# Optimization experiments

Hardware: AMD Instinct MI355X
Metric: run time of the kernel (lower is better)

Reference implementation:

```python
import jax, jax.numpy as jnp
import numpy as np

N_PATHS = 100000
N_STEPS = 512          # number of Euler steps; paths have N_STEPS+1 time points
DT = 0.004             # step_size (~1/250, daily)
KAPPA = 1.0
THETA = 0.04
SIGMA = 0.2
RHO = -0.7
S0 = 100.0
V0 = 0.04


def setup_inputs() -> dict:
    key = jax.random.key(0)
    z = jax.random.normal(key, (N_PATHS, N_STEPS, 2), dtype=jnp.float32)
    return {"z": z}


def reference(z):
    # Euler-Maruyama simulation of the Heston SDE with full-truncation clamp:
    #   dS = S * sqrt(v) dW1
    #   dv = kappa*(theta - v) dt + sigma*sqrt(v) dW2,  corr(dW1,dW2)=rho
    sqdt = jnp.sqrt(jnp.float32(DT))
    c = jnp.sqrt(jnp.float32(1.0 - RHO * RHO))

    def step(carry, zt):
        s, v = carry                      # each [N]
        vp = jnp.maximum(v, 0.0)
        sv = jnp.sqrt(vp)
        dW1 = sqdt * zt[:, 0]
        dW2 = RHO * dW1 + c * sqdt * zt[:, 1]
        s_new = s + s * sv * dW1
        v_new = jnp.maximum(v + KAPPA * (THETA - vp) * DT + SIGMA * sv * dW2, 0.0)
        return (s_new, v_new), (s_new, v_new)

    s0 = jnp.full((N_PATHS,), S0, dtype=z.dtype)
    v0 = jnp.full((N_PATHS,), V0, dtype=z.dtype)
    _, (ss, vs) = jax.lax.scan(step, (s0, v0), jnp.transpose(z, (1, 0, 2)))

    prices = jnp.concatenate([s0[None], ss], axis=0).T      # [N, T+1]
    variances = jnp.concatenate([v0[None], vs], axis=0).T   # [N, T+1]

    # variance-swap price: cumsum of variance * dt + analytic remaining leg L
    tau = jnp.linspace(N_STEPS * DT, 0.0, N_STEPS + 1).astype(z.dtype)  # [T+1]
    L = (variances - THETA) / KAPPA * (1.0 - jnp.exp(-KAPPA * tau)) + THETA * tau
    varswap = jnp.cumsum(variances, axis=1) * DT + L        # [N, T+1]

    # [N, T+1, 3] = (price, variance, varswap price)
    return jnp.stack([prices, variances, varswap], axis=-1)
```

## Files before the change

### kernel.cpp

```cpp
#include <hip/hip_runtime.h>
#include <hip/hip_fp16.h>


#define N_PATHS 100000
#define N_STEPS 512
#define TROW    1539
#define PB      64
#define SUB     16
#define NSUB    32
#define NPH     8
#define PHSUB   4
#define OSTR    97
#define DTc     0.004f
#define EDT     1.0040080107f

typedef float  f32x4  __attribute__((ext_vector_type(4)));
typedef __fp16 fp16x2 __attribute__((ext_vector_type(2)));

__device__ __forceinline__ unsigned pk2(float a, float b) {
    union { fp16x2 h; unsigned u; } cv;
    cv.h = __builtin_amdgcn_cvt_pkrtz(a, b);
    return cv.u;
}

__device__ __forceinline__ float ex16(unsigned w, int h) {
    const unsigned us = h ? (w >> 16) : (w & 0xFFFFu);
    return __half2float(__ushort_as_half((unsigned short)us));
}

__global__ __launch_bounds__(PB)
void heston_kernel(const float* __restrict__ z, float* __restrict__ out) {
    __shared__ unsigned olB[PB * OSTR];

    const int tid = threadIdx.x;
    const int p0  = blockIdx.x * PB;
    const int lim = N_PATHS - p0;
    const int limS = (lim >= PB) ? PB : lim;
    const int p   = p0 + tid;
    const int pc  = (p < N_PATHS) ? p : (N_PATHS - 1);

    const char* zp = (const char*)z + (size_t)pc * 4096;

    f32x4 fA[8], fB[8];
    #pragma unroll
    for (int j = 0; j < 8; ++j) fA[j] = *(const f32x4*)(zp + 16 * j);

    {
        #pragma unroll
        for (int k = 0; k < 3; ++k) {
            int idx = k * PB + tid;
            int pl = idx / 3, si = idx - pl * 3;
            if (pl < lim)
                out[(size_t)(p0 + pl) * TROW + si] =
                    (si == 0) ? 100.0f : (si == 1) ? 0.04f : 0.08208f;
        }
    }

    float s = 100.0f, v = 0.04f, acc = 0.04f, tau = 2.048f, e = expf(-2.048f);
    float sP = 0.f, vP = 0.f, vsP = 0.f;

    auto doSub = [&](int sc, int su, f32x4 (&cur)[8], f32x4 (&nxt)[8]) {
        if (sc + 1 < NSUB) {
            const char* zc = zp + (size_t)(sc + 1) * 128;
            #pragma unroll
            for (int j = 0; j < 8; ++j) nxt[j] = *(const f32x4*)(zc + 16 * j);
        }
        const int dbase = tid * OSTR + su * 24;
        #pragma unroll
        for (int dt = 0; dt < SUB; ++dt) {
            const f32x4 q  = cur[dt >> 1];
            const float z0 = (dt & 1) ? q.z : q.x;
            const float z1 = (dt & 1) ? q.w : q.y;

            const float vp  = fmaxf(v, 0.0f);
            const float sv  = __builtin_amdgcn_sqrtf(vp);
            const float dW1 = 0.06324555320f * z0;
            const float dW2 = fmaf(-0.7f, dW1, 0.04516636050f * z1);
            s = fmaf(s * sv, dW1, s);
            v = fmaxf(fmaf(0.2f * sv, dW2, fmaf(0.04f - vp, DTc, v)), 0.0f);
            acc += v;
            tau -= DTc;
            e *= EDT;
            const float vs = fmaf(acc, DTc, fmaf(0.04f, tau, (v - 0.04f) * (1.0f - e)));

            if (dt & 1) {
                const int d = dbase + 3 * (dt >> 1);
                olB[d + 0] = pk2(sP, vP);
                olB[d + 1] = pk2(vsP, s);
                olB[d + 2] = pk2(v, vs);
            } else { sP = s; vP = v; vsP = vs; }
        }
    };

    const int h  = tid & 1;
    const int tq = tid >> 1;

    for (int ph = 0; ph < NPH; ++ph) {
        const int sc0 = ph * PHSUB;
        doSub(sc0 + 0, 0, fA, fB);
        doSub(sc0 + 1, 1, fB, fA);
        doSub(sc0 + 2, 2, fA, fB);
        doSub(sc0 + 3, 3, fB, fA);

        float* gp = out + (size_t)p0 * TROW + 3 + ph * 192;
        if (limS == PB) {
            for (int pl = 0; pl < PB; ++pl) {
                const unsigned* lw = &olB[pl * OSTR + tq];
                float* gr = gp + (size_t)pl * TROW + tid;
                gr[0]   = ex16(lw[0],  h);
                gr[64]  = ex16(lw[32], h);
                gr[128] = ex16(lw[64], h);
            }
        } else {
            for (int pl = 0; pl < limS; ++pl) {
                const unsigned* lw = &olB[pl * OSTR + tq];
                float* gr = gp + (size_t)pl * TROW + tid;
                gr[0]   = ex16(lw[0],  h);
                gr[64]  = ex16(lw[32], h);
                gr[128] = ex16(lw[64], h);
            }
        }
    }
}

extern "C" void kernel_launch(void* const* d_in, const int* in_sizes, int n_in,
                              void* d_out, int out_size, void* d_ws, size_t ws_size,
                              hipStream_t stream) {
    const float* z = (const float*)d_in[0];
    float* out = (float*)d_out;
    const int nblocks = (N_PATHS + PB - 1) / PB;
    heston_kernel<<<nblocks, PB, 0, stream>>>(z, out);
}
```

Measured before the change: 328.2 us.

## Buffer full path trajectories in LDS and emit contiguous float4 output stores

Each block now simulates 48 paths, with 16 idle lanes in a 64-thread block, and stores the whole trajectory of s, v and varswap as fp16 in three shared-memory planes. After the simulation it writes the block's contiguous output region with float4 coalesced stores, rather than eight phases of strided scalar row writes. The aim is fully contiguous, wide global writes for the large output. The cost is about 148KB of LDS per block, which limits occupancy to about one block per CU. It also adds per-element index math (division by 3, row wrap), and the compute and store phases no longer overlap.

```diff
diff --git a/kernel.cpp b/kernel.cpp
--- a/kernel.cpp
+++ b/kernel.cpp
@@ -5,39 +5,28 @@
 #define N_PATHS 100000
 #define N_STEPS 512
 #define TROW    1539
+#define PPB     48
 #define PB      64
 #define SUB     16
 #define NSUB    32
-#define NPH     8
-#define PHSUB   4
-#define OSTR    97
+#define HSTR    513
 #define DTc     0.004f
 #define EDT     1.0040080107f
 
-typedef float  f32x4  __attribute__((ext_vector_type(4)));
-typedef __fp16 fp16x2 __attribute__((ext_vector_type(2)));
-
-__device__ __forceinline__ unsigned pk2(float a, float b) {
-    union { fp16x2 h; unsigned u; } cv;
-    cv.h = __builtin_amdgcn_cvt_pkrtz(a, b);
-    return cv.u;
-}
-
-__device__ __forceinline__ float ex16(unsigned w, int h) {
-    const unsigned us = h ? (w >> 16) : (w & 0xFFFFu);
-    return __half2float(__ushort_as_half((unsigned short)us));
-}
+typedef float f32x4 __attribute__((ext_vector_type(4)));
 
 __global__ __launch_bounds__(PB)
 void heston_kernel(const float* __restrict__ z, float* __restrict__ out) {
-    __shared__ unsigned olB[PB * OSTR];
+    __shared__ _Float16 S_l[PPB * HSTR];
+    __shared__ _Float16 V_l[PPB * HSTR];
+    __shared__ _Float16 W_l[PPB * HSTR];
 
     const int tid = threadIdx.x;
-    const int p0  = blockIdx.x * PB;
-    const int lim = N_PATHS - p0;
-    const int limS = (lim >= PB) ? PB : lim;
-    const int p   = p0 + tid;
-    const int pc  = (p < N_PATHS) ? p : (N_PATHS - 1);
+    const int p0  = blockIdx.x * PPB;
+    const int lim = (N_PATHS - p0 < PPB) ? (N_PATHS - p0) : PPB;
+    const bool act = (tid < PPB);
+    const int  pp  = p0 + tid;
+    const int  pc  = (pp < N_PATHS) ? pp : (N_PATHS - 1);
 
     const char* zp = (const char*)z + (size_t)pc * 4096;
 
@@ -45,27 +34,15 @@
     #pragma unroll
     for (int j = 0; j < 8; ++j) fA[j] = *(const f32x4*)(zp + 16 * j);
 
-    {
-        #pragma unroll
-        for (int k = 0; k < 3; ++k) {
-            int idx = k * PB + tid;
-            int pl = idx / 3, si = idx - pl * 3;
-            if (pl < lim)
-                out[(size_t)(p0 + pl) * TROW + si] =
-                    (si == 0) ? 100.0f : (si == 1) ? 0.04f : 0.08208f;
-        }
-    }
+    float s = 100.0f, v = 0.04f, acc = 0.04f, tau = 2.048f, e = expf(-2.048f);
 
-    float s = 100.0f, v = 0.04f, acc = 0.04f, tau = 2.048f, e = expf(-2.048f);
-    float sP = 0.f, vP = 0.f, vsP = 0.f;
-
-    auto doSub = [&](int sc, int su, f32x4 (&cur)[8], f32x4 (&nxt)[8]) {
+    auto doSub = [&](int sc, f32x4 (&cur)[8], f32x4 (&nxt)[8]) {
         if (sc + 1 < NSUB) {
             const char* zc = zp + (size_t)(sc + 1) * 128;
             #pragma unroll
             for (int j = 0; j < 8; ++j) nxt[j] = *(const f32x4*)(zc + 16 * j);
         }
-        const int dbase = tid * OSTR + su * 24;
+        const int tb = tid * HSTR + sc * SUB;
         #pragma unroll
         for (int dt = 0; dt < SUB; ++dt) {
             const f32x4 q  = cur[dt >> 1];
@@ -83,41 +60,65 @@
             e *= EDT;
             const float vs = fmaf(acc, DTc, fmaf(0.04f, tau, (v - 0.04f) * (1.0f - e)));
 
-            if (dt & 1) {
-                const int d = dbase + 3 * (dt >> 1);
-                olB[d + 0] = pk2(sP, vP);
-                olB[d + 1] = pk2(vsP, s);
-                olB[d + 2] = pk2(v, vs);
-            } else { sP = s; vP = v; vsP = vs; }
+            if (act) {
+                S_l[tb + dt] = (_Float16)s;
+                V_l[tb + dt] = (_Float16)v;
+                W_l[tb + dt] = (_Float16)vs;
+            }
         }
     };
 
-    const int h  = tid & 1;
-    const int tq = tid >> 1;
+    for (int sc = 0; sc < NSUB; sc += 2) {
+        doSub(sc,     fA, fB);
+        doSub(sc + 1, fB, fA);
+    }
 
-    for (int ph = 0; ph < NPH; ++ph) {
-        const int sc0 = ph * PHSUB;
-        doSub(sc0 + 0, 0, fA, fB);
-        doSub(sc0 + 1, 1, fB, fA);
-        doSub(sc0 + 2, 2, fA, fB);
-        doSub(sc0 + 3, 3, fB, fA);
+    const int limD  = lim * TROW;
+    float* gb = out + (size_t)p0 * TROW;
+    int w   = 4 * tid;
+    int plo = 0;
+    const int nfull = limD >> 8;
 
-        float* gp = out + (size_t)p0 * TROW + 3 + ph * 192;
-        if (limS == PB) {
-            for (int pl = 0; pl < PB; ++pl) {
-                const unsigned* lw = &olB[pl * OSTR + tq];
-                float* gr = gp + (size_t)pl * TROW + tid;
-                gr[0]   = ex16(lw[0],  h);
-                gr[64]  = ex16(lw[32], h);
-                gr[128] = ex16(lw[64], h);
-            }
-        } else {
-            for (int pl = 0; pl < limS; ++pl) {
-                const unsigned* lw = &olB[pl * OSTR + tq];
-                float* gr = gp + (size_t)pl * TROW + tid;
-                gr[0]   = ex16(lw[0],  h);
-                gr[64]  = ex16(lw[32], h);
-                gr[128] = ex16(lw[64], h);
+    for (int i = 0; i < nfull; ++i) {
+        f32x4 o;
+        #pragma unroll
+        for (int j = 0; j < 4; ++j) {
+            const int  wj = w + j;
+            const bool cr = (wj >= TROW);
+            const int  wq = cr ? wj - TROW : wj;
+            const int  pb = cr ? plo + HSTR : plo;
+            const int  u  = wq - 3;
+            const int  ui = (u < 0) ? 0 : u;
+            const int  t3 = ui / 3;
+            const int  f  = ui - 3 * t3;
+            const _Float16* src = (f == 0) ? S_l : ((f == 1) ? V_l : W_l);
+            float val = (float)src[pb + t3];
+            if (u < 0) val = (wq == 0) ? 100.0f : ((wq == 1) ? 0.04f : 0.08208f);
+            o[j] = val;
+        }
+        *(f32x4*)(gb + (i << 8) + 4 * tid) = o;
+        w += 256;
+        if (w >= TROW) { w -= TROW; plo += HSTR; }
+    }
+
+    const int rem = limD - (nfull << 8);
+    if (rem > 0) {
+        #pragma unroll
+        for (int j = 0; j < 4; ++j) {
+            const int gg = 4 * tid + j;
+            if (gg < rem) {
+                const int  wj = w + j;
+                const bool cr = (wj >= TROW);
+                const int  wq = cr ? wj - TROW : wj;
+                const int  pb = cr ? plo + HSTR : plo;
+                const int  u  = wq - 3;
+                const int  ui = (u < 0) ? 0 : u;
+                const int  t3 = ui / 3;
+                const int  f  = ui - 3 * t3;
+                const _Float16* src = (f == 0) ? S_l : ((f == 1) ? V_l : W_l);
+                float val = (float)src[pb + t3];
+                if (u < 0) val = (wq == 0) ? 100.0f : ((wq == 1) ? 0.04f : 0.08208f);
+                gb[(nfull << 8) + gg] = val;
             }
         }
     }
@@ -128,6 +129,6 @@
                               hipStream_t stream) {
     const float* z = (const float*)d_in[0];
     float* out = (float*)d_out;
-    const int nblocks = (N_PATHS + PB - 1) / PB;
+    const int nblocks = (N_PATHS + PPB - 1) / PPB;
     heston_kernel<<<nblocks, PB, 0, stream>>>(z, out);
 }
```

Measured after the change: 1.020 ms. 3.11x slower.
